# Optimization experiments

Hardware: AMD Instinct MI355X
Metric: run time of the kernel (lower is better)

Reference implementation:

```python
import jax, jax.numpy as jnp
import numpy as np

NUM_HEADS = 12
D_MODEL = 768
D_K = D_MODEL // NUM_HEADS
NEG_INF = -1e9  # matches torch masked_fill value -1000000000.0


def setup_inputs() -> dict:
    key = jax.random.key(0)
    ks = jax.random.split(key, 11)
    B, S, D = 2, 2048, D_MODEL
    s = 1.0 / np.sqrt(D)  # ~ nn.Linear default init scale
    return {
        "q": jax.random.normal(ks[0], (B, S, D), jnp.float32),
        "k": jax.random.normal(ks[1], (B, S, D), jnp.float32),
        "v": jax.random.normal(ks[2], (B, S, D), jnp.float32),
        "mask": jax.random.randint(ks[3], (B, S, S), 0, 2, jnp.int32),
        "Wq": jax.random.normal(ks[4], (D, D), jnp.float32) * s,
        "bq": jax.random.normal(ks[5], (D,), jnp.float32) * s,
        "Wk": jax.random.normal(ks[6], (D, D), jnp.float32) * s,
        "bk": jax.random.normal(ks[7], (D,), jnp.float32) * s,
        "Wv": jax.random.normal(ks[8], (D, D), jnp.float32) * s,
        "bv": jax.random.normal(ks[9], (D,), jnp.float32) * s,
    }


def reference(q, k, v, mask, Wq, bq, Wk, bk, Wv, bv):
    B, S, D = q.shape
    H, dk = NUM_HEADS, D_K
    # torch nn.Linear: x @ W.T + b, then .view(B, H, -1, d_k)
    # NOTE: source uses a raw view (NO transpose) -> plain reshape here, faithfully.
    qh = (q @ Wq.T + bq).reshape(B, H, S, dk)
    kh = (k @ Wk.T + bk).reshape(B, H, S, dk)
    vh = (v @ Wv.T + bv).reshape(B, H, S, dk)
    scores = jnp.einsum("bhqd,bhkd->bhqk", qh, kh) / jnp.sqrt(jnp.asarray(dk, q.dtype))
    # mask.unsqueeze(1): broadcast over heads; masked_fill where mask == 0
    scores = jnp.where(mask[:, None, :, :] == 0, jnp.asarray(NEG_INF, q.dtype), scores)
    attn = jax.nn.softmax(scores, axis=-1)  # dropout = identity (eval mode)
    return jnp.einsum("bhqk,bhkd->bhqd", attn, vh)  # (B, H, S, d_k); no out-proj in source
```

## Files before the change

### kernel.cpp

```cpp
#include <hip/hip_runtime.h>
#include <stdint.h>

#define NUM_B 2
#define SEQ 2048
#define DMODEL 768
#define NHEAD 12
#define DK 64
#define MROWS (NUM_B * SEQ)
#define BHS (NUM_B * NHEAD * SEQ)

typedef __attribute__((ext_vector_type(4))) float f32x4;
typedef __attribute__((ext_vector_type(16))) float f32x16;
typedef __attribute__((ext_vector_type(8))) short bf16x8;
typedef __attribute__((ext_vector_type(8))) unsigned short us8;
typedef __attribute__((ext_vector_type(4))) unsigned int u32x4;
typedef unsigned short u16;
typedef unsigned int u32;
typedef unsigned long long u64;

__device__ __forceinline__ u16 to_bf16(float f) {
  u32 u = __builtin_bit_cast(u32, f);
  u += 0x7FFFu + ((u >> 16) & 1u);
  return (u16)(u >> 16);
}

__device__ __forceinline__ u32 cvt_pk_bf16(float lo, float hi) {
  u32 r;
  asm("v_cvt_pk_bf16_f32 %0, %1, %2" : "=v"(r) : "v"(lo), "v"(hi));
  return r;
}

__device__ __forceinline__ void gload_lds16(const u16* g, u16* l) {
#pragma clang diagnostic push
#pragma clang diagnostic ignored "-Waddress-space-conversion"
  __builtin_amdgcn_global_load_lds((const __attribute__((address_space(1))) u32*)g,
                                   (__attribute__((address_space(3))) u32*)l, 16, 0, 0);
#pragma clang diagnostic pop
}

__global__ void cvt_kernel(const float* s0, const float* s1, const float* s2,
                           const float* s3, const float* s4, const float* s5,
                           u16* d0, u16* d1, u16* d2, u16* d3, u16* d4, u16* d5,
                           int nbig, int nsmall) {
  int y = blockIdx.y;
  const float* src; u16* dst; int n8;
  if (y == 0)      { src = s0; dst = d0; n8 = nbig; }
  else if (y == 1) { src = s1; dst = d1; n8 = nbig; }
  else if (y == 2) { src = s2; dst = d2; n8 = nbig; }
  else if (y == 3) { src = s3; dst = d3; n8 = nsmall; }
  else if (y == 4) { src = s4; dst = d4; n8 = nsmall; }
  else             { src = s5; dst = d5; n8 = nsmall; }
  int i = blockIdx.x * blockDim.x + threadIdx.x;
  if (i >= n8) return;
  const f32x4* p = reinterpret_cast<const f32x4*>(src) + (size_t)i * 2;
  f32x4 lo = p[0], hi = p[1];
  us8 r;
  r[0] = to_bf16(lo[0]); r[1] = to_bf16(lo[1]); r[2] = to_bf16(lo[2]); r[3] = to_bf16(lo[3]);
  r[4] = to_bf16(hi[0]); r[5] = to_bf16(hi[1]); r[6] = to_bf16(hi[2]); r[7] = to_bf16(hi[3]);
  *(reinterpret_cast<us8*>(dst) + i) = r;
}

__global__ void pack_mask(const int* __restrict__ mask, u64* __restrict__ bits) {
  int i = blockIdx.x * 256 + threadIdx.x;
  int m = mask[i];
  u64 bm = __ballot(m != 0);
  if ((threadIdx.x & 63) == 0) {
    int word = (i >> 6) & 31;
    int s = (i >> 11) & 2047;
    int b = i >> 22;
    bits[((size_t)b * 32 + word) * 2048 + s] = bm;
  }
}

__global__ __launch_bounds__(256) void proj_gemm(
    const u16* __restrict__ X0, const u16* __restrict__ X1, const u16* __restrict__ X2,
    const u16* __restrict__ W0, const u16* __restrict__ W1, const u16* __restrict__ W2,
    const float* __restrict__ b0, const float* __restrict__ b1, const float* __restrict__ b2,
    u16* __restrict__ o0, u16* __restrict__ o1, u16* __restrict__ o2) {
  __shared__ u16 As[2][8192];
  __shared__ u16 Bs[2][8192];

  int lin = blockIdx.x + 192 * blockIdx.y;
  int wid = (lin & 7) * 72 + (lin >> 3);
  int y = wid / 192;
  int r192 = wid % 192;
  int bm = r192 / 6, bn = r192 % 6;

  const u16* X; const u16* W; const float* bias; u16* out;
  if (y == 0)      { X = X0; W = W0; bias = b0; out = o0; }
  else if (y == 1) { X = X1; W = W1; bias = b1; out = o1; }
  else             { X = X2; W = W2; bias = b2; out = o2; }
  float osc = (y == 0) ? 0.18033688011112042f : 1.0f;

  int tid = threadIdx.x, w = tid >> 6, l = tid & 63;
  int g = l >> 4, c = l & 15;
  int m0 = bm * 128, n0 = bn * 128;
  int wm = w >> 1, wn = w & 1;

  int srow = l >> 3;
  int cg = (l & 7) ^ srow;

  f32x4 acc[4][4] = {};

  auto stage = [&](int kt, int buf) {
    int k0 = kt * 64;
#pragma unroll
    for (int i = 0; i < 4; ++i) {
      int row = i * 32 + w * 8 + srow;
      gload_lds16(X + (size_t)(m0 + row) * DMODEL + k0 + cg * 8, &As[buf][(i * 256 + w * 64) * 8]);
    }
#pragma unroll
    for (int i = 0; i < 4; ++i) {
      int row = i * 32 + w * 8 + srow;
      gload_lds16(W + (size_t)(n0 + row) * DMODEL + k0 + cg * 8, &Bs[buf][(i * 256 + w * 64) * 8]);
    }
  };

  stage(0, 0);
  __syncthreads();

  for (int kt = 0; kt < 12; ++kt) {
    int cur = kt & 1;
    if (kt < 11) stage(kt + 1, cur ^ 1);
#pragma unroll
    for (int kk = 0; kk < 2; ++kk) {
      bf16x8 av[4], bv[4];
#pragma unroll
      for (int m = 0; m < 4; ++m) {
        int row = wm * 64 + m * 16 + c;
        av[m] = *(const bf16x8*)&As[cur][row * 64 + ((kk * 32 + g * 8) ^ ((row & 7) << 3))];
      }
#pragma unroll
      for (int n = 0; n < 4; ++n) {
        int row = wn * 64 + n * 16 + c;
        bv[n] = *(const bf16x8*)&Bs[cur][row * 64 + ((kk * 32 + g * 8) ^ ((row & 7) << 3))];
      }
#pragma unroll
      for (int m = 0; m < 4; ++m)
#pragma unroll
        for (int n = 0; n < 4; ++n)
          acc[m][n] = __builtin_amdgcn_mfma_f32_16x16x32_bf16(av[m], bv[n], acc[m][n], 0, 0, 0);
    }
    __syncthreads();
  }
#pragma unroll
  for (int n = 0; n < 4; ++n) {
    int gcol = n0 + wn * 64 + n * 16 + c;
    float bvv = bias[gcol];
#pragma unroll
    for (int m = 0; m < 4; ++m) {
      int grow0 = m0 + wm * 64 + m * 16 + g * 4;
#pragma unroll
      for (int r = 0; r < 4; ++r)
        out[(size_t)(grow0 + r) * DMODEL + gcol] = to_bf16((acc[m][n][r] + bvv) * osc);
    }
  }
}

__global__ __launch_bounds__(256) void transposeV(const u16* __restrict__ vh,
                                                  u16* __restrict__ vhT) {
  __shared__ u16 T[64][72];
  int bh = blockIdx.y;
  int s0 = blockIdx.x * 64;
  int tid = threadIdx.x;
#pragma unroll
  for (int it = 0; it < 2; ++it) {
    int cch = it * 256 + tid;
    int r = cch >> 3, dc = (cch & 7) * 8;
    us8 v = *(const us8*)(vh + ((size_t)bh * 2048 + s0 + r) * 64 + dc);
#pragma unroll
    for (int j = 0; j < 8; ++j) T[dc + j][r] = v[j];
  }
  __syncthreads();
#pragma unroll
  for (int it = 0; it < 2; ++it) {
    int cch = it * 256 + tid;
    int d = cch >> 3, sc = (cch & 7) * 8;
    us8 v = *(const us8*)&T[d][sc];
    *(us8*)(vhT + ((size_t)bh * 64 + d) * 2048 + s0 + sc) = v;
  }
}

__global__ __launch_bounds__(256) void attn32(
    const u16* __restrict__ qh, const u16* __restrict__ kh, const u16* __restrict__ vt,
    const u64* __restrict__ mbt, float* __restrict__ po0, float* __restrict__ po1,
    float* __restrict__ pl) {
  __shared__ u16 K0[4096], V0[4096], K1[4096], V1[4096];

  int tid = threadIdx.x, w = tid >> 6, l = tid & 63;
  int q = l & 31, hi = l >> 5;

  int lin = blockIdx.x + 16 * (blockIdx.y + 12 * blockIdx.z);
  int wid = (lin & 7) * 96 + (lin >> 3);
  int qb = wid & 15;
  int rest = wid >> 4;
  int h = rest % 12;
  int z = rest / 12;
  int b = z >> 1, strip = z & 1;
  int kbase = strip * 1024;
  size_t hb = (size_t)(b * NHEAD + h) * SEQ * DK;
  int qrow = qb * 128 + w * 32 + q;

  bf16x8 qf[4];
#pragma unroll
  for (int s = 0; s < 4; ++s)
    qf[s] = *(const bf16x8*)(qh + hb + (size_t)qrow * DK + s * 16 + hi * 8);

  f32x16 o0 = {}, o1 = {};
  float l_run = 0.f;

  int idx0 = w * 64 + l;
  int r0s = idx0 >> 3;
  int sc0 = ((idx0 & 7) ^ (r0s & 7)) * 8;
  const u16* kS = kh + hb + (size_t)(kbase + r0s) * DK + sc0;
  const u16* vS = vt + hb + (size_t)r0s * SEQ + kbase + sc0;
  const u64* mp = mbt + ((size_t)b * 32 + strip * 16) * SEQ + qrow;

  auto stage = [&](int t, u16* Kd, u16* Vd) {
    const u16* kp = kS + (size_t)t * (64 * DK);
    const u16* vp = vS + t * 64;
    gload_lds16(kp,            Kd + w * 512);
    gload_lds16(kp + 32 * DK,  Kd + 2048 + w * 512);
    gload_lds16(vp,            Vd + w * 512);
    gload_lds16(vp + 32 * SEQ, Vd + 2048 + w * 512);
  };

  int ofA[4];
#pragma unroll
  for (int s = 0; s < 4; ++s)
    ofA[s] = q * 64 + (((2 * s + hi) ^ (q & 7)) * 8);

  auto compute = [&](const u16* Kc, const u16* Vc, u64 mcur) {
    f32x16 s0 = {}, s1 = {};
    __builtin_amdgcn_s_setprio(1);
#pragma unroll
    for (int s = 0; s < 4; ++s) {
      bf16x8 k0 = *(const bf16x8*)(Kc + ofA[s]);
      bf16x8 k1 = *(const bf16x8*)(Kc + ofA[s] + 2048);
      s0 = __builtin_amdgcn_mfma_f32_32x32x16_bf16(k0, qf[s], s0, 0, 0, 0);
      s1 = __builtin_amdgcn_mfma_f32_32x32x16_bf16(k1, qf[s], s1, 0, 0, 0);
    }
    __builtin_amdgcn_s_setprio(0);

    u32 mm0 = (u32)(mcur >> (4 * hi));
    u32 mm1 = (u32)((mcur >> 32) >> (4 * hi));
    float rs0 = 0.f, rs1 = 0.f;
#pragma unroll
    for (int r = 0; r < 16; ++r) {
      const int p = (r & 3) + 8 * (r >> 2);
      float e0 = exp2f(s0[r]);
      float e1 = exp2f(s1[r]);
      int k0m = ((int)(mm0 << (31 - p))) >> 31;
      int k1m = ((int)(mm1 << (31 - p))) >> 31;
      e0 = __builtin_bit_cast(float, __builtin_bit_cast(int, e0) & k0m);
      e1 = __builtin_bit_cast(float, __builtin_bit_cast(int, e1) & k1m);
      s0[r] = e0; s1[r] = e1;
      rs0 += e0; rs1 += e1;
    }
    l_run += rs0 + rs1;

#pragma unroll
    for (int kb = 0; kb < 2; ++kb) {
#pragma unroll
      for (int hf = 0; hf < 2; ++hf) {
        int ks = kb * 2 + hf;
        u32 A0, A1, B0, B1;
        if (kb == 0) {
          A0 = cvt_pk_bf16(s0[8 * hf + 0], s0[8 * hf + 1]);
          A1 = cvt_pk_bf16(s0[8 * hf + 2], s0[8 * hf + 3]);
          B0 = cvt_pk_bf16(s0[8 * hf + 4], s0[8 * hf + 5]);
          B1 = cvt_pk_bf16(s0[8 * hf + 6], s0[8 * hf + 7]);
        } else {
          A0 = cvt_pk_bf16(s1[8 * hf + 0], s1[8 * hf + 1]);
          A1 = cvt_pk_bf16(s1[8 * hf + 2], s1[8 * hf + 3]);
          B0 = cvt_pk_bf16(s1[8 * hf + 4], s1[8 * hf + 5]);
          B1 = cvt_pk_bf16(s1[8 * hf + 6], s1[8 * hf + 7]);
        }
        u32 z0 = hi ? A0 : B0;
        u32 z1 = hi ? A1 : B1;
        u32 sw0 = __shfl_xor(z0, 32);
        u32 sw1 = __shfl_xor(z1, 32);
        u32x4 fw;
        fw[0] = hi ? sw0 : A0;
        fw[1] = hi ? sw1 : A1;
        fw[2] = hi ? B0 : sw0;
        fw[3] = hi ? B1 : sw1;
        bf16x8 pa = __builtin_bit_cast(bf16x8, fw);
        bf16x8 v0 = *(const bf16x8*)(Vc + ofA[ks]);
        bf16x8 v1 = *(const bf16x8*)(Vc + ofA[ks] + 2048);
        __builtin_amdgcn_s_setprio(1);
        o0 = __builtin_amdgcn_mfma_f32_32x32x16_bf16(pa, v0, o0, 0, 0, 0);
        o1 = __builtin_amdgcn_mfma_f32_32x32x16_bf16(pa, v1, o1, 0, 0, 0);
        __builtin_amdgcn_s_setprio(0);
      }
    }
  };

  stage(0, K0, V0);
  u64 mcur = mp[0];
  __syncthreads();

  for (int tt = 0; tt < 8; ++tt) {
    const int t0 = 2 * tt;
    u64 mnext = mp[(size_t)(t0 + 1) * SEQ];
    stage(t0 + 1, K1, V1);
    compute(K0, V0, mcur);
    __syncthreads();
    mcur = mnext;
    if (tt < 7) {
      mnext = mp[(size_t)(t0 + 2) * SEQ];
      stage(t0 + 2, K0, V0);
    }
    compute(K1, V1, mcur);
    __syncthreads();
    mcur = mnext;
  }

  l_run += __shfl_xor(l_run, 32);
  float* oo = strip ? po1 : po0;
#pragma unroll
  for (int r = 0; r < 16; ++r) {
    int row = qb * 128 + w * 32 + (r & 3) + 8 * (r >> 2) + 4 * hi;
    oo[hb + (size_t)row * DK + q]      = o0[r];
    oo[hb + (size_t)row * DK + 32 + q] = o1[r];
  }
  if (hi == 0) {
    size_t rowg = (size_t)(b * NHEAD + h) * SEQ + qrow;
    pl[(size_t)strip * BHS + rowg] = l_run;
  }
}

__global__ __launch_bounds__(256) void combine_kernel(
    const float* __restrict__ po0, const float* __restrict__ po1,
    const float* __restrict__ pl, float* __restrict__ out) {
  int i = blockIdx.x * 256 + threadIdx.x;
  int row = i >> 4;
  float l0 = pl[row], l1 = pl[BHS + row];
  float inv = 1.f / (l0 + l1);
  f32x4 a = ((const f32x4*)po0)[i];
  f32x4 b = ((const f32x4*)po1)[i];
  ((f32x4*)out)[i] = (a + b) * inv;
}

extern "C" void kernel_launch(void* const* d_in, const int* in_sizes, int n_in,
                              void* d_out, int out_size, void* d_ws, size_t ws_size,
                              hipStream_t stream) {
  const float* q    = (const float*)d_in[0];
  const float* k    = (const float*)d_in[1];
  const float* v    = (const float*)d_in[2];
  const int*   mask = (const int*)d_in[3];
  const float* Wq   = (const float*)d_in[4];
  const float* bq   = (const float*)d_in[5];
  const float* Wk   = (const float*)d_in[6];
  const float* bk   = (const float*)d_in[7];
  const float* Wv   = (const float*)d_in[8];
  const float* bv   = (const float*)d_in[9];

  char* ws = (char*)d_ws;
  const size_t szX = (size_t)MROWS * DMODEL * 2;
  const size_t szW = (size_t)DMODEL * DMODEL * 2;
  u16* xq  = (u16*)(ws);
  u16* xk  = (u16*)(ws + szX);
  u16* xv  = (u16*)(ws + 2 * szX);
  u16* wqb = (u16*)(ws + 3 * szX);
  u16* wkb = (u16*)(ws + 3 * szX + szW);
  u16* wvb = (u16*)(ws + 3 * szX + 2 * szW);
  u16* qh  = (u16*)(ws + 3 * szX + 3 * szW);
  u16* kh  = (u16*)(ws + 4 * szX + 3 * szW);
  u16* vh  = (u16*)(ws + 5 * szX + 3 * szW);
  u64* mb  = (u64*)(ws + 6 * szX + 3 * szW);

  float* po1 = (float*)(ws);
  u16*   vhT = (u16*)(ws + 2 * szX);
  float* pl  = (float*)(ws + 3 * szX);
  float* po0 = (float*)d_out;

  const int nbig = (MROWS * DMODEL) / 8;
  const int nsmall = (DMODEL * DMODEL) / 8;

  cvt_kernel<<<dim3(1536, 6), 256, 0, stream>>>(q, k, v, Wq, Wk, Wv,
                                                xq, xk, xv, wqb, wkb, wvb, nbig, nsmall);
  pack_mask<<<(NUM_B * SEQ * SEQ) / 256, 256, 0, stream>>>(mask, mb);
  proj_gemm<<<dim3(192, 3), 256, 0, stream>>>(
      xq, xk, xv, wqb, wkb, wvb, bq, bk, bv, qh, kh, vh);
  transposeV<<<dim3(32, 24), 256, 0, stream>>>(vh, vhT);
  attn32<<<dim3(16, 12, 4), 256, 0, stream>>>(qh, kh, vhT, mb, po0, po1, pl);
  combine_kernel<<<(BHS * 16) / 256, 256, 0, stream>>>(po0, po1, pl, (float*)d_out);
}
```

Baseline: 125.5 us.

## Fuse mask packing into convert kernel, compute row sums via MFMA, use permlane32 swap

Merges the mask bit-packing launch into the fp32-to-bf16 convert kernel as an extra grid row, removing one kernel launch. In the attention kernel, row sums of probabilities are now computed by an extra MFMA against a ones vector instead of scalar adds plus a cross-lane shuffle. The half-wave exchange of packed P fragments uses v_permlane32_swap instead of __shfl_xor with selects. Risks: the extra MFMA per step adds matrix-unit work, the row sum now comes from bf16-rounded P (which does match what multiplies V), and the convert grid grows to 2048 blocks, with most of them idle for the weight rows.

After: 116.6 us. 1.08x faster.

```diff
diff --git a/kernel.cpp b/kernel.cpp
--- a/kernel.cpp
+++ b/kernel.cpp
@@ -38,11 +38,27 @@
 #pragma clang diagnostic pop
 }
 
-__global__ void cvt_kernel(const float* s0, const float* s1, const float* s2,
-                           const float* s3, const float* s4, const float* s5,
-                           u16* d0, u16* d1, u16* d2, u16* d3, u16* d4, u16* d5,
-                           int nbig, int nsmall) {
+__global__ void cvt_pack(const float* s0, const float* s1, const float* s2,
+                         const float* s3, const float* s4, const float* s5,
+                         const int* __restrict__ mask,
+                         u16* d0, u16* d1, u16* d2, u16* d3, u16* d4, u16* d5,
+                         u64* __restrict__ bits, int nbig, int nsmall) {
   int y = blockIdx.y;
+  if (y == 6) {
+    int base = blockIdx.x * (16 * 256) + threadIdx.x;
+#pragma unroll
+    for (int it = 0; it < 16; ++it) {
+      int i = base + it * 256;
+      u64 bm = __ballot(mask[i] != 0);
+      if ((threadIdx.x & 63) == 0) {
+        int word = (i >> 6) & 31;
+        int s = (i >> 11) & 2047;
+        int b = i >> 22;
+        bits[((size_t)b * 32 + word) * 2048 + s] = bm;
+      }
+    }
+    return;
+  }
   const float* src; u16* dst; int n8;
   if (y == 0)      { src = s0; dst = d0; n8 = nbig; }
   else if (y == 1) { src = s1; dst = d1; n8 = nbig; }
@@ -60,18 +76,6 @@
   *(reinterpret_cast<us8*>(dst) + i) = r;
 }
 
-__global__ void pack_mask(const int* __restrict__ mask, u64* __restrict__ bits) {
-  int i = blockIdx.x * 256 + threadIdx.x;
-  int m = mask[i];
-  u64 bm = __ballot(m != 0);
-  if ((threadIdx.x & 63) == 0) {
-    int word = (i >> 6) & 31;
-    int s = (i >> 11) & 2047;
-    int b = i >> 22;
-    bits[((size_t)b * 32 + word) * 2048 + s] = bm;
-  }
-}
-
 __global__ __launch_bounds__(256) void proj_gemm(
     const u16* __restrict__ X0, const u16* __restrict__ X1, const u16* __restrict__ X2,
     const u16* __restrict__ W0, const u16* __restrict__ W1, const u16* __restrict__ W2,
@@ -206,8 +210,11 @@
   for (int s = 0; s < 4; ++s)
     qf[s] = *(const bf16x8*)(qh + hb + (size_t)qrow * DK + s * 16 + hi * 8);
 
-  f32x16 o0 = {}, o1 = {};
-  float l_run = 0.f;
+  bf16x8 ones;
+#pragma unroll
+  for (int j = 0; j < 8; ++j) ones[j] = (short)0x3F80;
+
+  f32x16 o0 = {}, o1 = {}, o_l = {};
 
   int idx0 = w * 64 + l;
   int r0s = idx0 >> 3;
@@ -244,7 +251,6 @@
 
     u32 mm0 = (u32)(mcur >> (4 * hi));
     u32 mm1 = (u32)((mcur >> 32) >> (4 * hi));
-    float rs0 = 0.f, rs1 = 0.f;
 #pragma unroll
     for (int r = 0; r < 16; ++r) {
       const int p = (r & 3) + 8 * (r >> 2);
@@ -252,12 +258,9 @@
       float e1 = exp2f(s1[r]);
       int k0m = ((int)(mm0 << (31 - p))) >> 31;
       int k1m = ((int)(mm1 << (31 - p))) >> 31;
-      e0 = __builtin_bit_cast(float, __builtin_bit_cast(int, e0) & k0m);
-      e1 = __builtin_bit_cast(float, __builtin_bit_cast(int, e1) & k1m);
-      s0[r] = e0; s1[r] = e1;
-      rs0 += e0; rs1 += e1;
-    }
-    l_run += rs0 + rs1;
+      s0[r] = __builtin_bit_cast(float, __builtin_bit_cast(int, e0) & k0m);
+      s1[r] = __builtin_bit_cast(float, __builtin_bit_cast(int, e1) & k1m);
+    }
 
 #pragma unroll
     for (int kb = 0; kb < 2; ++kb) {
@@ -276,21 +279,17 @@
           B0 = cvt_pk_bf16(s1[8 * hf + 4], s1[8 * hf + 5]);
           B1 = cvt_pk_bf16(s1[8 * hf + 6], s1[8 * hf + 7]);
         }
-        u32 z0 = hi ? A0 : B0;
-        u32 z1 = hi ? A1 : B1;
-        u32 sw0 = __shfl_xor(z0, 32);
-        u32 sw1 = __shfl_xor(z1, 32);
+        asm("v_permlane32_swap_b32 %0, %1" : "+v"(A0), "+v"(B0));
+        asm("v_permlane32_swap_b32 %0, %1" : "+v"(A1), "+v"(B1));
         u32x4 fw;
-        fw[0] = hi ? sw0 : A0;
-        fw[1] = hi ? sw1 : A1;
-        fw[2] = hi ? B0 : sw0;
-        fw[3] = hi ? B1 : sw1;
+        fw[0] = A0; fw[1] = A1; fw[2] = B0; fw[3] = B1;
         bf16x8 pa = __builtin_bit_cast(bf16x8, fw);
         bf16x8 v0 = *(const bf16x8*)(Vc + ofA[ks]);
         bf16x8 v1 = *(const bf16x8*)(Vc + ofA[ks] + 2048);
         __builtin_amdgcn_s_setprio(1);
         o0 = __builtin_amdgcn_mfma_f32_32x32x16_bf16(pa, v0, o0, 0, 0, 0);
         o1 = __builtin_amdgcn_mfma_f32_32x32x16_bf16(pa, v1, o1, 0, 0, 0);
+        o_l = __builtin_amdgcn_mfma_f32_32x32x16_bf16(pa, ones, o_l, 0, 0, 0);
         __builtin_amdgcn_s_setprio(0);
       }
     }
@@ -316,7 +315,6 @@
     mcur = mnext;
   }
 
-  l_run += __shfl_xor(l_run, 32);
   float* oo = strip ? po1 : po0;
 #pragma unroll
   for (int r = 0; r < 16; ++r) {
@@ -324,9 +322,11 @@
     oo[hb + (size_t)row * DK + q]      = o0[r];
     oo[hb + (size_t)row * DK + 32 + q] = o1[r];
   }
-  if (hi == 0) {
-    size_t rowg = (size_t)(b * NHEAD + h) * SEQ + qrow;
-    pl[(size_t)strip * BHS + rowg] = l_run;
+  if (q == 0) {
+    size_t base2 = (size_t)(b * NHEAD + h) * SEQ + qb * 128 + w * 32 + 4 * hi;
+#pragma unroll
+    for (int r = 0; r < 16; ++r)
+      pl[(size_t)strip * BHS + base2 + (r & 3) + 8 * (r >> 2)] = o_l[r];
   }
 }
 
@@ -378,9 +378,9 @@
   const int nbig = (MROWS * DMODEL) / 8;
   const int nsmall = (DMODEL * DMODEL) / 8;
 
-  cvt_kernel<<<dim3(1536, 6), 256, 0, stream>>>(q, k, v, Wq, Wk, Wv,
-                                                xq, xk, xv, wqb, wkb, wvb, nbig, nsmall);
-  pack_mask<<<(NUM_B * SEQ * SEQ) / 256, 256, 0, stream>>>(mask, mb);
+  cvt_pack<<<dim3(2048, 7), 256, 0, stream>>>(q, k, v, Wq, Wk, Wv, mask,
+                                              xq, xk, xv, wqb, wkb, wvb, mb,
+                                              nbig, nsmall);
   proj_gemm<<<dim3(192, 3), 256, 0, stream>>>(
       xq, xk, xv, wqb, wkb, wvb, bq, bk, bv, qh, kh, vh);
   transposeV<<<dim3(32, 24), 256, 0, stream>>>(vh, vhT);
```
